# Performance work log

Hardware: AMD Instinct MI355X
Metric: run time of the kernel (lower is better)

## Reference

```python
import jax, jax.numpy as jnp
import numpy as np

DECAY = 0.99
EPSILON = 1e-05
BETA = 0.25  # vq_commitment_beta


def setup_inputs() -> dict:
    key = jax.random.key(0)
    k1, k2, k3, k4 = jax.random.split(key, 4)
    N, dim, K = 32768, 512, 8192
    init_range = 1.0 / np.sqrt(dim)
    emb_w = jax.random.uniform(k3, (K, 2 * dim), dtype=jnp.float32,
                               minval=-init_range, maxval=init_range)
    return {
        "z_real": jax.random.normal(k1, (N, dim), dtype=jnp.float32),
        "z_imag": jax.random.normal(k2, (N, dim), dtype=jnp.float32),
        "emb_w": emb_w,
        "ema_cluster_size": jnp.zeros((K,), dtype=jnp.float32),
        "ema_w": emb_w.copy(),
    }


def reference(z_real, z_imag, emb_w, ema_cluster_size, ema_w):
    N, dim = z_real.shape
    K = emb_w.shape[0]
    z_flat = jnp.concatenate([z_real, z_imag], axis=-1)  # [N, 2*dim]

    # squared euclidean distances [N, K]
    x_sq = jnp.sum(z_flat * z_flat, axis=1, keepdims=True)
    y_sq = jnp.sum(emb_w * emb_w, axis=1)
    d = jnp.maximum(x_sq + y_sq - 2.0 * (z_flat @ emb_w.T), 0.0)
    indices = jnp.argmin(d, axis=-1)  # [N]
    z_q = emb_w[indices]              # [N, 2*dim]

    # EMA codebook update (training-mode buffer math, no grads)
    n_total = jnp.zeros((K,), z_flat.dtype).at[indices].add(1.0)
    new_cluster_size = ema_cluster_size * DECAY + (1.0 - DECAY) * n_total
    cs = new_cluster_size + EPSILON
    cs = cs + (cs < 1.0).astype(cs.dtype)
    dw = jnp.zeros((K, 2 * dim), z_flat.dtype).at[indices].add(z_flat)  # encodings.T @ z_flat
    new_ema_w = ema_w * DECAY + (1.0 - DECAY) * dw
    new_w = jnp.clip(new_ema_w / cs[:, None], -5.0, 5.0)

    loss_sample = BETA * jnp.mean((z_q - z_flat) ** 2, axis=-1)  # [N]

    # straight-through (forward value == z_q)
    z_q_st = z_flat + jax.lax.stop_gradient(z_q - z_flat)

    probs = n_total / N
    norm_entropy = -jnp.sum(probs * jnp.log(probs + 1e-10)) / np.log(float(K))

    z_q_r = z_q_st[..., :dim]
    z_q_i = z_q_st[..., dim:]
    return (z_q_r, z_q_i, loss_sample, indices, norm_entropy,
            new_w, new_cluster_size, new_ema_w)
```

## Files before the change

### kernel.cpp

```cpp
#include <hip/hip_runtime.h>
#include <hip/hip_bf16.h>

#define NROWS 32768
#define DIM   512
#define D2    1024
#define KCODE 8192
#define DECAYF 0.99f
#define OMD    0.01f
#define CANDCAP 16
#define ZMAX 6.0f
#define IRANGE 0.04419417382415922f
#define MARGIN_I 9200

typedef __attribute__((ext_vector_type(4))) float f32x4;
typedef __attribute__((ext_vector_type(4))) int   v4i;
typedef __attribute__((ext_vector_type(16))) int  i32x16;

#define WS_EMB8T   0u
#define WS_YSQ     8388608u
#define WS_NINT    8421376u
#define WS_ENT     8454144u
#define WS_CCOUNT  8454160u
#define WS_CAND    8585232u
#define WS_FIDX    10682384u
#define WS_OFF     10813456u
#define WS_CUR     10846224u
#define WS_ROWLIST 10878992u

#define OUT_ZQR  0
#define OUT_ZQI  16777216
#define OUT_LOSS 33554432
#define OUT_IDX  33587200
#define OUT_ENT  33619968
#define OUT_NEWW 33619969
#define OUT_NCS  42008577
#define OUT_NEMA 42016769

__device__ __forceinline__ float wredf(float v) {
    #pragma unroll
    for (int o = 32; o > 0; o >>= 1) v += __shfl_down(v, o, 64);
    return v;
}

__device__ __forceinline__ double wredd(double v) {
    #pragma unroll
    for (int o = 32; o > 0; o >>= 1) v += __shfl_down(v, o, 64);
    return __shfl(v, 0, 64);
}

__device__ __forceinline__ double ulp32_of(double v) {
    return scalbn(1.0, ilogb(v) - 23);
}

__device__ __forceinline__ void gload_lds16(const void* g, void* l) {
    __builtin_amdgcn_global_load_lds(
        (const __attribute__((address_space(1))) unsigned int*)(g),
        (__attribute__((address_space(3))) unsigned int*)(l), 16, 0, 0);
}

__device__ __forceinline__ int q4(float4 v, float s) {
    int a = (int)rintf(fminf(fmaxf(v.x * s, -127.f), 127.f));
    int b = (int)rintf(fminf(fmaxf(v.y * s, -127.f), 127.f));
    int c = (int)rintf(fminf(fmaxf(v.z * s, -127.f), 127.f));
    int d = (int)rintf(fminf(fmaxf(v.w * s, -127.f), 127.f));
    return (a & 255) | ((b & 255) << 8) | ((c & 255) << 16) | ((d & 255) << 24);
}

__global__ __launch_bounds__(256) void prep_emb(const float* __restrict__ emb,
                                                char* __restrict__ emb8t,
                                                int* __restrict__ ysq) {
    int wave = threadIdx.x >> 6, lane = threadIdx.x & 63;
    int k = blockIdx.x * 4 + wave;
    const float4* src = (const float4*)(emb + (size_t)k * D2);
    const float es = 127.0f / IRANGE;
    const float sfac_inv = 1.0f / (2.0f * (ZMAX / 127.0f) * (IRANGE / 127.0f));
    float s = 0.f;
    float4 v0 = src[lane * 4 + 0];
    float4 v1 = src[lane * 4 + 1];
    float4 v2 = src[lane * 4 + 2];
    float4 v3 = src[lane * 4 + 3];
    s += v0.x*v0.x + v0.y*v0.y + v0.z*v0.z + v0.w*v0.w;
    s += v1.x*v1.x + v1.y*v1.y + v1.z*v1.z + v1.w*v1.w;
    s += v2.x*v2.x + v2.y*v2.y + v2.z*v2.z + v2.w*v2.w;
    s += v3.x*v3.x + v3.y*v3.y + v3.z*v3.z + v3.w*v3.w;
    v4i pk; pk[0] = q4(v0, es); pk[1] = q4(v1, es); pk[2] = q4(v2, es); pk[3] = q4(v3, es);
    v4i* dst = (v4i*)(emb8t + (size_t)(k >> 5) * 32768 + (size_t)lane * 512 + (k & 31) * 16);
    *dst = pk;
    s = wredf(s);
    if (lane == 0) ysq[k] = (int)rintf(s * sfac_inv);
}

__global__ __launch_bounds__(512, 2) void argmin_gemm(
    const float* __restrict__ zr, const float* __restrict__ zi,
    const char* __restrict__ emb8t, const int* __restrict__ ysq,
    long long* __restrict__ pairs)
{
    __shared__ char bufs[2][65536];
    const int tid  = threadIdx.x;
    const int wave = tid >> 6, lane = tid & 63;
    const int colc = lane & 31;
    const int hh   = lane >> 5;
    const int rowblk = blockIdx.x >> 1;
    const int slice  = blockIdx.x & 1;

    const int arow = rowblk * 256 + wave * 32 + colc;
    const float zs = 127.0f / ZMAX;
    const float* zrp = zr + (size_t)arow * 512 + hh * 16;
    const float* zip = zi + (size_t)arow * 512 + hh * 16;
    v4i afrag[32];
    #pragma unroll
    for (int ft = 0; ft < 16; ++ft) {
        const float4* p = (const float4*)(zrp + ft * 32);
        v4i a; a[0] = q4(p[0], zs); a[1] = q4(p[1], zs); a[2] = q4(p[2], zs); a[3] = q4(p[3], zs);
        afrag[ft] = a;
    }
    #pragma unroll
    for (int ft = 0; ft < 16; ++ft) {
        const float4* p = (const float4*)(zip + ft * 32);
        v4i a; a[0] = q4(p[0], zs); a[1] = q4(p[1], zs); a[2] = q4(p[2], zs); a[3] = q4(p[3], zs);
        afrag[16 + ft] = a;
    }

    int tv0[16], tv1[16], cpk[16];
    #pragma unroll
    for (int g = 0; g < 16; ++g) { tv0[g] = 0x7FFFFFFF; tv1[g] = 0x7FFFFFFF; cpk[g] = 0; }

    const char* gslice = emb8t + (size_t)slice * 128 * 32768;
    const int* yslice = ysq + slice * 4096;

#define STAGE(dstbuf, c_) do {                                                   \
        const char* gb = gslice + (size_t)(c_) * 65536 + wave * 8192             \
                       + (size_t)lane * 16;                                      \
        char* lb = (dstbuf) + wave * 8192;                                       \
        _Pragma("unroll")                                                        \
        for (int q = 0; q < 8; ++q)                                              \
            gload_lds16(gb + q * 1024, lb + q * 1024);                           \
    } while (0)

    const int boff = colc * 16 + hh * 512;

    STAGE(bufs[0], 0);
    __syncthreads();

    for (int c = 0; c < 64; ++c) {
        const int cur = c & 1;
        if (c + 1 < 64) STAGE(bufs[cur ^ 1], c + 1);

        const char* bb = &bufs[cur][0] + boff;
        i32x16 accA, accB;
        #pragma unroll
        for (int g = 0; g < 16; ++g) { accA[g] = 0; accB[g] = 0; }
        #pragma unroll
        for (int m = 0; m < 32; ++m) {
            v4i bA = *(const v4i*)(bb + m * 1024);
            v4i bB = *(const v4i*)(bb + m * 1024 + 32768);
            accA = __builtin_amdgcn_mfma_i32_32x32x32_i8(afrag[m], bA, accA, 0, 0, 0);
            accB = __builtin_amdgcn_mfma_i32_32x32x32_i8(afrag[m], bB, accB, 0, 0, 0);
        }

        int ysA = yslice[c * 64 + colc];
        int ysB = yslice[c * 64 + 32 + colc];
        const int idA = c * 2, idB = c * 2 + 1;
        #pragma unroll
        for (int g = 0; g < 16; ++g) {
            int sc = ysA - accA[g];
            if (sc < tv1[g]) {
                bool b0 = sc < tv0[g];
                int cp = cpk[g];
                cpk[g] = b0 ? (((cp & 0xFF) << 8) | idA) : ((cp & 0xFF) | (idA << 8));
                int ov0 = tv0[g];
                tv1[g] = b0 ? ov0 : sc;
                tv0[g] = b0 ? sc : ov0;
            }
            sc = ysB - accB[g];
            if (sc < tv1[g]) {
                bool b0 = sc < tv0[g];
                int cp = cpk[g];
                cpk[g] = b0 ? (((cp & 0xFF) << 8) | idB) : ((cp & 0xFF) | (idB << 8));
                int ov0 = tv0[g];
                tv1[g] = b0 ? ov0 : sc;
                tv0[g] = b0 ? sc : ov0;
            }
        }
        __syncthreads();
    }
#undef STAGE

    #pragma unroll
    for (int g = 0; g < 16; ++g) {
        int rloc = (g & 3) + 8 * (g >> 2) + 4 * hh;
        int rowg = rowblk * 256 + wave * 32 + rloc;
        size_t base = (size_t)rowg * 128 + slice * 64 + colc * 2;
        int cp = cpk[g];
        int code0 = slice * 4096 + (cp & 0xFF) * 32 + colc;
        int code1 = slice * 4096 + ((cp >> 8) & 0xFF) * 32 + colc;
        pairs[base + 0] = ((long long)(unsigned)code0 << 32) | (unsigned)tv0[g];
        pairs[base + 1] = ((long long)(unsigned)code1 << 32) | (unsigned)tv1[g];
    }
}

__global__ __launch_bounds__(256) void merge_rows(const long long* __restrict__ pairs,
                                                  int* __restrict__ cand,
                                                  int* __restrict__ ccount)
{
    int wave = threadIdx.x >> 6, lane = threadIdx.x & 63;
    int row = blockIdx.x * 4 + wave;
    const long long* pr = pairs + (size_t)row * 128;
    long long p0 = pr[lane];
    long long p1 = pr[64 + lane];
    int v0v = (int)(unsigned)p0;
    int i0  = (int)(p0 >> 32);
    int v1v = (int)(unsigned)p1;
    int i1  = (int)(p1 >> 32);
    int m = min(v0v, v1v);
    #pragma unroll
    for (int o = 32; o > 0; o >>= 1) m = min(m, __shfl_xor(m, o, 64));
    int lim = m + MARGIN_I;
    unsigned long long m0 = __ballot(v0v < lim);
    unsigned long long m1 = __ballot(v1v < lim);
    int t0 = __popcll(m0);
    int cnt = t0 + __popcll(m1);
    if (cnt > CANDCAP) cnt = CANDCAP;
    unsigned long long below = (lane == 63) ? 0xFFFFFFFFFFFFFFFFull >> 1
                                            : ((1ull << lane) - 1);
    if (v0v < lim) {
        int pos = __popcll(m0 & below);
        if (pos < CANDCAP) cand[(size_t)row * CANDCAP + pos] = i0;
    }
    if (v1v < lim) {
        int pos = t0 + __popcll(m1 & below);
        if (pos < CANDCAP) cand[(size_t)row * CANDCAP + pos] = i1;
    }
    if (lane == 0) ccount[row] = cnt;
}

__global__ __launch_bounds__(256) void cleanup(
    const float* __restrict__ zr, const float* __restrict__ zi,
    const float* __restrict__ emb, const int* __restrict__ cand,
    const int* __restrict__ ccount, int* __restrict__ fidx,
    int* __restrict__ nint, float* __restrict__ out)
{
    int wave = threadIdx.x >> 6, lane = threadIdx.x & 63;
    int r = blockIdx.x * 4 + wave;
    int cnt = ccount[r];
    int best = cand[r * CANDCAP];

    float zreg[16];
    #pragma unroll
    for (int p = 0; p < 4; ++p) {
        int d4 = p * 64 + lane;
        const float4* zp = (d4 < 128) ? (const float4*)(zr + (size_t)r * 512)
                                      : ((const float4*)(zi + (size_t)r * 512) - 128);
        float4 zv = zp[d4];
        zreg[p * 4 + 0] = zv.x; zreg[p * 4 + 1] = zv.y;
        zreg[p * 4 + 2] = zv.z; zreg[p * 4 + 3] = zv.w;
    }

    if (cnt > 1) {
        double xs = 0.0;
        #pragma unroll
        for (int j = 0; j < 16; ++j) xs += (double)zreg[j] * (double)zreg[j];
        xs = wredd(xs);
        double uS = ulp32_of(xs);

        double bD = 1e300; int bi = 1 << 30;
        for (int i = 0; i < cnt; ++i) {
            int cdx = cand[r * CANDCAP + i];
            const float4* ep = (const float4*)(emb + (size_t)cdx * 1024);
            double ys = 0.0, tt = 0.0;
            #pragma unroll
            for (int p = 0; p < 4; ++p) {
                float4 ev = ep[p * 64 + lane];
                float p0 = ev.x * ev.x, p1 = ev.y * ev.y, p2 = ev.z * ev.z, p3 = ev.w * ev.w;
                ys += (double)p0 + (double)p1 + (double)p2 + (double)p3;
                tt += (double)zreg[p * 4 + 0] * (double)ev.x
                    + (double)zreg[p * 4 + 1] * (double)ev.y
                    + (double)zreg[p * 4 + 2] * (double)ev.z
                    + (double)zreg[p * 4 + 3] * (double)ev.w;
            }
            ys = wredd(ys);
            tt = wredd(tt);
            float y32 = (float)ys;
            float t32 = (float)tt;
            double dex = xs + ys - 2.0 * tt;
            double ud = ulp32_of(dex);
            double D = rint((double)y32 / uS) * uS - rint(2.0 * (double)t32 / ud) * ud;
            if (D < bD || (D == bD && cdx < bi)) { bD = D; bi = cdx; }
        }
        best = bi;
    }

    const float4* ep = (const float4*)(emb + (size_t)best * 1024);
    float acc = 0.f;
    #pragma unroll
    for (int p = 0; p < 4; ++p) {
        int d4 = p * 64 + lane;
        float4 ev = ep[d4];
        float dx = ev.x - zreg[p * 4 + 0]; acc += dx * dx;
        float dy = ev.y - zreg[p * 4 + 1]; acc += dy * dy;
        float dz = ev.z - zreg[p * 4 + 2]; acc += dz * dz;
        float dw = ev.w - zreg[p * 4 + 3]; acc += dw * dw;
        float4* op = (d4 < 128) ? (float4*)(out + OUT_ZQR + (size_t)r * 512)
                                : ((float4*)(out + OUT_ZQI + (size_t)r * 512) - 128);
        op[d4] = ev;
    }
    acc = wredf(acc);
    if (lane == 0) {
        fidx[r] = best;
        out[OUT_IDX + r] = (float)best;
        out[OUT_LOSS + r] = 0.25f * acc * (1.f / 1024.f);
        atomicAdd(nint + best, 1);
    }
}

__global__ __launch_bounds__(256) void scan_codes(const int* __restrict__ nint,
                                                  int* __restrict__ off,
                                                  int* __restrict__ cur) {
    __shared__ int part[256];
    int tid = threadIdx.x;
    int base = tid * 32;
    int loc[32];
    int s = 0;
    #pragma unroll
    for (int j = 0; j < 32; ++j) { loc[j] = s; s += nint[base + j]; }
    part[tid] = s;
    __syncthreads();
    for (int o = 1; o < 256; o <<= 1) {
        int t = (tid >= o) ? part[tid - o] : 0;
        __syncthreads();
        part[tid] += t;
        __syncthreads();
    }
    int excl = part[tid] - s;
    #pragma unroll
    for (int j = 0; j < 32; ++j) {
        off[base + j] = excl + loc[j];
        cur[base + j] = 0;
    }
}

__global__ __launch_bounds__(256) void fill_rows(const int* __restrict__ fidx,
                                                 const int* __restrict__ off,
                                                 int* __restrict__ cur,
                                                 int* __restrict__ rowlist) {
    int r = blockIdx.x * 256 + threadIdx.x;
    int idx = fidx[r];
    int pos = atomicAdd(cur + idx, 1);
    rowlist[off[idx] + pos] = r;
}

__global__ __launch_bounds__(256) void ema_update(
    const float* __restrict__ zr, const float* __restrict__ zi,
    const float* __restrict__ emaw, const float* __restrict__ emacs,
    const int* __restrict__ nint, const int* __restrict__ off,
    const int* __restrict__ rowlist, float* __restrict__ out,
    float* __restrict__ entacc)
{
    int k = blockIdx.x;
    int tid = threadIdx.x;
    int cnt = nint[k];
    int o0 = off[k];
    float ax = 0.f, ay = 0.f, az = 0.f, aw = 0.f;
    for (int i = 0; i < cnt; ++i) {
        int r = rowlist[o0 + i];
        float4 zv = (tid < 128) ? ((const float4*)(zr + (size_t)r * 512))[tid]
                                : ((const float4*)(zi + (size_t)r * 512))[tid - 128];
        ax += zv.x; ay += zv.y; az += zv.z; aw += zv.w;
    }
    float4 ew = ((const float4*)(emaw + (size_t)k * 1024))[tid];
    float4 nem;
    nem.x = DECAYF * ew.x + OMD * ax;
    nem.y = DECAYF * ew.y + OMD * ay;
    nem.z = DECAYF * ew.z + OMD * az;
    nem.w = DECAYF * ew.w + OMD * aw;
    ((float4*)(out + OUT_NEMA + (size_t)k * 1024))[tid] = nem;
    float ncs = DECAYF * emacs[k] + OMD * (float)cnt;
    float cs = ncs + 1e-5f;
    if (cs < 1.f) cs += 1.f;
    float inv = 1.f / cs;
    float4 w;
    w.x = fminf(fmaxf(nem.x * inv, -5.f), 5.f);
    w.y = fminf(fmaxf(nem.y * inv, -5.f), 5.f);
    w.z = fminf(fmaxf(nem.z * inv, -5.f), 5.f);
    w.w = fminf(fmaxf(nem.w * inv, -5.f), 5.f);
    ((float4*)(out + OUT_NEWW + (size_t)k * 1024))[tid] = w;
    if (tid == 0) {
        out[OUT_NCS + k] = ncs;
        float p = (float)cnt / 32768.f;
        atomicAdd(entacc, -p * logf(p + 1e-10f));
    }
}

__global__ void ent_fin(const float* __restrict__ entacc, float* __restrict__ out) {
    if (threadIdx.x == 0) out[OUT_ENT] = entacc[0] / logf(8192.f);
}

extern "C" void kernel_launch(void* const* d_in, const int* in_sizes, int n_in,
                              void* d_out, int out_size, void* d_ws, size_t ws_size,
                              hipStream_t stream)
{
    const float* zr    = (const float*)d_in[0];
    const float* zi    = (const float*)d_in[1];
    const float* emb   = (const float*)d_in[2];
    const float* emacs = (const float*)d_in[3];
    const float* emaw  = (const float*)d_in[4];
    float* out = (float*)d_out;
    char* ws = (char*)d_ws;

    char*  emb8t   = (char*)(ws + WS_EMB8T);
    int*   ysq     = (int*)(ws + WS_YSQ);
    int*   nint    = (int*)(ws + WS_NINT);
    float* entacc  = (float*)(ws + WS_ENT);
    int*   ccount  = (int*)(ws + WS_CCOUNT);
    int*   cand    = (int*)(ws + WS_CAND);
    int*   fidx    = (int*)(ws + WS_FIDX);
    int*   off     = (int*)(ws + WS_OFF);
    int*   cur     = (int*)(ws + WS_CUR);
    int*   rowlist = (int*)(ws + WS_ROWLIST);
    long long* pairs = (long long*)out;

    hipMemsetAsync(ws + WS_NINT, 0, 32768 + 16, stream);

    prep_emb   <<<2048, 256, 0, stream>>>(emb, emb8t, ysq);
    argmin_gemm<<<256,  512, 0, stream>>>(zr, zi, emb8t, ysq, pairs);
    merge_rows <<<8192, 256, 0, stream>>>(pairs, cand, ccount);
    cleanup    <<<8192, 256, 0, stream>>>(zr, zi, emb, cand, ccount, fidx, nint, out);
    scan_codes <<<1,    256, 0, stream>>>(nint, off, cur);
    fill_rows  <<<128,  256, 0, stream>>>(fidx, off, cur, rowlist);
    ema_update <<<8192, 256, 0, stream>>>(zr, zi, emaw, emacs, nint, off, rowlist, out, entacc);
    ent_fin    <<<1,    64,  0, stream>>>(entacc, out);
}
```

Baseline: 550.9 us.

## Software-pipeline top-2 selection behind next chunk's MFMAs with packed branchless keys

The distance-scan kernel now double-buffers its MFMA accumulators, so each chunk's top-2 update runs on the previous chunk's results and can overlap the current chunk's matrix instructions. The top-2 tracking becomes branchless by packing the chunk id into the low 7 bits of a shifted score and using min/max, which removes the separate cpk index register. It also raises wave priority around the MFMA block with s_setprio. The cost is a second set of accumulators, which adds register pressure. The shifted score could overflow if distances are large, and the merge margin is rescaled to match the new key format.

Result: slower. 1.871 ms (+239.6%).

```diff
diff --git a/kernel.cpp b/kernel.cpp
--- a/kernel.cpp
+++ b/kernel.cpp
@@ -10,9 +10,8 @@
 #define CANDCAP 16
 #define ZMAX 6.0f
 #define IRANGE 0.04419417382415922f
-#define MARGIN_I 9200
-
-typedef __attribute__((ext_vector_type(4))) float f32x4;
+#define MARGIN_P (9200 << 7)
+
 typedef __attribute__((ext_vector_type(4))) int   v4i;
 typedef __attribute__((ext_vector_type(16))) int  i32x16;
 
@@ -121,9 +120,9 @@
         afrag[16 + ft] = a;
     }
 
-    int tv0[16], tv1[16], cpk[16];
-    #pragma unroll
-    for (int g = 0; g < 16; ++g) { tv0[g] = 0x7FFFFFFF; tv1[g] = 0x7FFFFFFF; cpk[g] = 0; }
+    int tv0[16], tv1[16];
+    #pragma unroll
+    for (int g = 0; g < 16; ++g) { tv0[g] = 0x7FFFFFFF; tv1[g] = 0x7FFFFFFF; }
 
     const char* gslice = emb8t + (size_t)slice * 128 * 32768;
     const int* yslice = ysq + slice * 4096;
@@ -139,63 +138,76 @@
 
     const int boff = colc * 16 + hh * 512;
 
+    i32x16 accA0, accB0, accA1, accB1;
+    #pragma unroll
+    for (int g = 0; g < 16; ++g) { accA1[g] = 0; accB1[g] = 0; }
+    int pysA = 1 << 23, pysB = 1 << 23, pidA = 0, pidB = 0;
+
     STAGE(bufs[0], 0);
     __syncthreads();
 
-    for (int c = 0; c < 64; ++c) {
-        const int cur = c & 1;
-        if (c + 1 < 64) STAGE(bufs[cur ^ 1], c + 1);
-
-        const char* bb = &bufs[cur][0] + boff;
-        i32x16 accA, accB;
-        #pragma unroll
-        for (int g = 0; g < 16; ++g) { accA[g] = 0; accB[g] = 0; }
-        #pragma unroll
-        for (int m = 0; m < 32; ++m) {
-            v4i bA = *(const v4i*)(bb + m * 1024);
-            v4i bB = *(const v4i*)(bb + m * 1024 + 32768);
-            accA = __builtin_amdgcn_mfma_i32_32x32x32_i8(afrag[m], bA, accA, 0, 0, 0);
-            accB = __builtin_amdgcn_mfma_i32_32x32x32_i8(afrag[m], bB, accB, 0, 0, 0);
-        }
-
-        int ysA = yslice[c * 64 + colc];
-        int ysB = yslice[c * 64 + 32 + colc];
-        const int idA = c * 2, idB = c * 2 + 1;
-        #pragma unroll
-        for (int g = 0; g < 16; ++g) {
-            int sc = ysA - accA[g];
-            if (sc < tv1[g]) {
-                bool b0 = sc < tv0[g];
-                int cp = cpk[g];
-                cpk[g] = b0 ? (((cp & 0xFF) << 8) | idA) : ((cp & 0xFF) | (idA << 8));
-                int ov0 = tv0[g];
-                tv1[g] = b0 ? ov0 : sc;
-                tv0[g] = b0 ? sc : ov0;
-            }
-            sc = ysB - accB[g];
-            if (sc < tv1[g]) {
-                bool b0 = sc < tv0[g];
-                int cp = cpk[g];
-                cpk[g] = b0 ? (((cp & 0xFF) << 8) | idB) : ((cp & 0xFF) | (idB << 8));
-                int ov0 = tv0[g];
-                tv1[g] = b0 ? ov0 : sc;
-                tv0[g] = b0 ? sc : ov0;
-            }
-        }
-        __syncthreads();
-    }
+#define CHUNK_BODY(c_, curA, curB, prvA, prvB) do {                              \
+        const int cc = (c_);                                                     \
+        if (cc + 1 < 64) STAGE(bufs[(cc + 1) & 1], cc + 1);                      \
+        const char* bb = &bufs[cc & 1][0] + boff;                                \
+        _Pragma("unroll")                                                        \
+        for (int g = 0; g < 16; ++g) { curA[g] = 0; curB[g] = 0; }               \
+        __builtin_amdgcn_s_setprio(1);                                           \
+        _Pragma("unroll")                                                        \
+        for (int m = 0; m < 32; ++m) {                                           \
+            v4i bA = *(const v4i*)(bb + m * 1024);                               \
+            v4i bB = *(const v4i*)(bb + m * 1024 + 32768);                       \
+            curA = __builtin_amdgcn_mfma_i32_32x32x32_i8(afrag[m], bA, curA, 0, 0, 0); \
+            curB = __builtin_amdgcn_mfma_i32_32x32x32_i8(afrag[m], bB, curB, 0, 0, 0); \
+        }                                                                        \
+        __builtin_amdgcn_s_setprio(0);                                           \
+        _Pragma("unroll")                                                        \
+        for (int g = 0; g < 16; ++g) {                                           \
+            int pkA = ((pysA - prvA[g]) << 7) | pidA;                            \
+            int t1A = min(tv1[g], max(pkA, tv0[g]));                             \
+            tv0[g] = min(tv0[g], pkA);                                           \
+            tv1[g] = t1A;                                                        \
+            int pkB = ((pysB - prvB[g]) << 7) | pidB;                            \
+            int t1B = min(tv1[g], max(pkB, tv0[g]));                             \
+            tv0[g] = min(tv0[g], pkB);                                           \
+            tv1[g] = t1B;                                                        \
+        }                                                                        \
+        pysA = yslice[cc * 64 + colc];                                           \
+        pysB = yslice[cc * 64 + 32 + colc];                                      \
+        pidA = cc * 2;                                                           \
+        pidB = cc * 2 + 1;                                                       \
+        __syncthreads();                                                         \
+    } while (0)
+
+    for (int cp = 0; cp < 32; ++cp) {
+        CHUNK_BODY(2 * cp,     accA0, accB0, accA1, accB1);
+        CHUNK_BODY(2 * cp + 1, accA1, accB1, accA0, accB0);
+    }
+#undef CHUNK_BODY
 #undef STAGE
+
+    #pragma unroll
+    for (int g = 0; g < 16; ++g) {
+        int pkA = ((pysA - accA1[g]) << 7) | pidA;
+        int t1A = min(tv1[g], max(pkA, tv0[g]));
+        tv0[g] = min(tv0[g], pkA);
+        tv1[g] = t1A;
+        int pkB = ((pysB - accB1[g]) << 7) | pidB;
+        int t1B = min(tv1[g], max(pkB, tv0[g]));
+        tv0[g] = min(tv0[g], pkB);
+        tv1[g] = t1B;
+    }
 
     #pragma unroll
     for (int g = 0; g < 16; ++g) {
         int rloc = (g & 3) + 8 * (g >> 2) + 4 * hh;
         int rowg = rowblk * 256 + wave * 32 + rloc;
         size_t base = (size_t)rowg * 128 + slice * 64 + colc * 2;
-        int cp = cpk[g];
-        int code0 = slice * 4096 + (cp & 0xFF) * 32 + colc;
-        int code1 = slice * 4096 + ((cp >> 8) & 0xFF) * 32 + colc;
-        pairs[base + 0] = ((long long)(unsigned)code0 << 32) | (unsigned)tv0[g];
-        pairs[base + 1] = ((long long)(unsigned)code1 << 32) | (unsigned)tv1[g];
+        int t0 = tv0[g], t1 = tv1[g];
+        int code0 = slice * 4096 + (t0 & 127) * 32 + colc;
+        int code1 = slice * 4096 + (t1 & 127) * 32 + colc;
+        pairs[base + 0] = ((long long)(unsigned)code0 << 32) | (unsigned)t0;
+        pairs[base + 1] = ((long long)(unsigned)code1 << 32) | (unsigned)t1;
     }
 }
 
@@ -215,7 +227,7 @@
     int m = min(v0v, v1v);
     #pragma unroll
     for (int o = 32; o > 0; o >>= 1) m = min(m, __shfl_xor(m, o, 64));
-    int lim = m + MARGIN_I;
+    int lim = m + MARGIN_P;
     unsigned long long m0 = __ballot(v0v < lim);
     unsigned long long m1 = __ballot(v1v < lim);
     int t0 = __popcll(m0);
```

## Pack score and index for branchless top-2 and fuse merge into cleanup

Applied to the files above, without the earlier changes.

The GEMM epilogue now packs each int8 distance score with its 7-bit chunk index into a single int, so the top-2 tracking becomes branchless min/max operations instead of compare-and-select with a separate index word. The merge_rows kernel is folded into cleanup, which keeps the candidate list in LDS rather than round-tripping cand/ccount through global memory. The pairs buffer moves to the new_w region of the output so cleanup can write z_q outputs without clobbering it. MFMA loops are also wrapped in s_setprio and the ysq loads are hoisted ahead of the MFMAs. The shift by 7 risks overflow if scores exceed about 2^24, and ties now resolve by chunk index.

Result: faster. 518.1 us (-5.9%).

```diff
diff --git a/kernel.cpp b/kernel.cpp
--- a/kernel.cpp
+++ b/kernel.cpp
@@ -10,9 +10,8 @@
 #define CANDCAP 16
 #define ZMAX 6.0f
 #define IRANGE 0.04419417382415922f
-#define MARGIN_I 9200
-
-typedef __attribute__((ext_vector_type(4))) float f32x4;
+#define MARGIN_P (9200 << 7)
+
 typedef __attribute__((ext_vector_type(4))) int   v4i;
 typedef __attribute__((ext_vector_type(16))) int  i32x16;
 
@@ -20,8 +19,6 @@
 #define WS_YSQ     8388608u
 #define WS_NINT    8421376u
 #define WS_ENT     8454144u
-#define WS_CCOUNT  8454160u
-#define WS_CAND    8585232u
 #define WS_FIDX    10682384u
 #define WS_OFF     10813456u
 #define WS_CUR     10846224u
@@ -35,6 +32,7 @@
 #define OUT_NEWW 33619969
 #define OUT_NCS  42008577
 #define OUT_NEMA 42016769
+#define PAIRS_OFF (OUT_NEWW + 1)
 
 __device__ __forceinline__ float wredf(float v) {
     #pragma unroll
@@ -121,9 +119,9 @@
         afrag[16 + ft] = a;
     }
 
-    int tv0[16], tv1[16], cpk[16];
-    #pragma unroll
-    for (int g = 0; g < 16; ++g) { tv0[g] = 0x7FFFFFFF; tv1[g] = 0x7FFFFFFF; cpk[g] = 0; }
+    int tv0[16], tv1[16];
+    #pragma unroll
+    for (int g = 0; g < 16; ++g) { tv0[g] = 0x7FFFFFFF; tv1[g] = 0x7FFFFFFF; }
 
     const char* gslice = emb8t + (size_t)slice * 128 * 32768;
     const int* yslice = ysq + slice * 4096;
@@ -145,11 +143,14 @@
     for (int c = 0; c < 64; ++c) {
         const int cur = c & 1;
         if (c + 1 < 64) STAGE(bufs[cur ^ 1], c + 1);
+        int ysA = yslice[c * 64 + colc];
+        int ysB = yslice[c * 64 + 32 + colc];
 
         const char* bb = &bufs[cur][0] + boff;
         i32x16 accA, accB;
         #pragma unroll
         for (int g = 0; g < 16; ++g) { accA[g] = 0; accB[g] = 0; }
+        __builtin_amdgcn_s_setprio(1);
         #pragma unroll
         for (int m = 0; m < 32; ++m) {
             v4i bA = *(const v4i*)(bb + m * 1024);
@@ -157,30 +158,17 @@
             accA = __builtin_amdgcn_mfma_i32_32x32x32_i8(afrag[m], bA, accA, 0, 0, 0);
             accB = __builtin_amdgcn_mfma_i32_32x32x32_i8(afrag[m], bB, accB, 0, 0, 0);
         }
-
-        int ysA = yslice[c * 64 + colc];
-        int ysB = yslice[c * 64 + 32 + colc];
+        __builtin_amdgcn_s_setprio(0);
+
         const int idA = c * 2, idB = c * 2 + 1;
         #pragma unroll
         for (int g = 0; g < 16; ++g) {
-            int sc = ysA - accA[g];
-            if (sc < tv1[g]) {
-                bool b0 = sc < tv0[g];
-                int cp = cpk[g];
-                cpk[g] = b0 ? (((cp & 0xFF) << 8) | idA) : ((cp & 0xFF) | (idA << 8));
-                int ov0 = tv0[g];
-                tv1[g] = b0 ? ov0 : sc;
-                tv0[g] = b0 ? sc : ov0;
-            }
-            sc = ysB - accB[g];
-            if (sc < tv1[g]) {
-                bool b0 = sc < tv0[g];
-                int cp = cpk[g];
-                cpk[g] = b0 ? (((cp & 0xFF) << 8) | idB) : ((cp & 0xFF) | (idB << 8));
-                int ov0 = tv0[g];
-                tv1[g] = b0 ? ov0 : sc;
-                tv0[g] = b0 ? sc : ov0;
-            }
+            int pkA = ((ysA - accA[g]) << 7) | idA;
+            tv1[g] = min(tv1[g], max(pkA, tv0[g]));
+            tv0[g] = min(tv0[g], pkA);
+            int pkB = ((ysB - accB[g]) << 7) | idB;
+            tv1[g] = min(tv1[g], max(pkB, tv0[g]));
+            tv0[g] = min(tv0[g], pkB);
         }
         __syncthreads();
     }
@@ -191,21 +179,24 @@
         int rloc = (g & 3) + 8 * (g >> 2) + 4 * hh;
         int rowg = rowblk * 256 + wave * 32 + rloc;
         size_t base = (size_t)rowg * 128 + slice * 64 + colc * 2;
-        int cp = cpk[g];
-        int code0 = slice * 4096 + (cp & 0xFF) * 32 + colc;
-        int code1 = slice * 4096 + ((cp >> 8) & 0xFF) * 32 + colc;
-        pairs[base + 0] = ((long long)(unsigned)code0 << 32) | (unsigned)tv0[g];
-        pairs[base + 1] = ((long long)(unsigned)code1 << 32) | (unsigned)tv1[g];
-    }
-}
-
-__global__ __launch_bounds__(256) void merge_rows(const long long* __restrict__ pairs,
-                                                  int* __restrict__ cand,
-                                                  int* __restrict__ ccount)
+        int t0 = tv0[g], t1 = tv1[g];
+        int code0 = slice * 4096 + (t0 & 127) * 32 + colc;
+        int code1 = slice * 4096 + (t1 & 127) * 32 + colc;
+        pairs[base + 0] = ((long long)(unsigned)code0 << 32) | (unsigned)t0;
+        pairs[base + 1] = ((long long)(unsigned)code1 << 32) | (unsigned)t1;
+    }
+}
+
+__global__ __launch_bounds__(256) void cleanup(
+    const float* __restrict__ zr, const float* __restrict__ zi,
+    const float* __restrict__ emb, const long long* __restrict__ pairs,
+    int* __restrict__ fidx, int* __restrict__ nint, float* __restrict__ out)
 {
+    __shared__ int candlds[4][CANDCAP];
     int wave = threadIdx.x >> 6, lane = threadIdx.x & 63;
-    int row = blockIdx.x * 4 + wave;
-    const long long* pr = pairs + (size_t)row * 128;
+    int r = blockIdx.x * 4 + wave;
+
+    const long long* pr = pairs + (size_t)r * 128;
     long long p0 = pr[lane];
     long long p1 = pr[64 + lane];
     int v0v = (int)(unsigned)p0;
@@ -215,7 +206,7 @@
     int m = min(v0v, v1v);
     #pragma unroll
     for (int o = 32; o > 0; o >>= 1) m = min(m, __shfl_xor(m, o, 64));
-    int lim = m + MARGIN_I;
+    int lim = m + MARGIN_P;
     unsigned long long m0 = __ballot(v0v < lim);
     unsigned long long m1 = __ballot(v1v < lim);
     int t0 = __popcll(m0);
@@ -225,25 +216,13 @@
                                             : ((1ull << lane) - 1);
     if (v0v < lim) {
         int pos = __popcll(m0 & below);
-        if (pos < CANDCAP) cand[(size_t)row * CANDCAP + pos] = i0;
+        if (pos < CANDCAP) candlds[wave][pos] = i0;
     }
     if (v1v < lim) {
         int pos = t0 + __popcll(m1 & below);
-        if (pos < CANDCAP) cand[(size_t)row * CANDCAP + pos] = i1;
-    }
-    if (lane == 0) ccount[row] = cnt;
-}
-
-__global__ __launch_bounds__(256) void cleanup(
-    const float* __restrict__ zr, const float* __restrict__ zi,
-    const float* __restrict__ emb, const int* __restrict__ cand,
-    const int* __restrict__ ccount, int* __restrict__ fidx,
-    int* __restrict__ nint, float* __restrict__ out)
-{
-    int wave = threadIdx.x >> 6, lane = threadIdx.x & 63;
-    int r = blockIdx.x * 4 + wave;
-    int cnt = ccount[r];
-    int best = cand[r * CANDCAP];
+        if (pos < CANDCAP) candlds[wave][pos] = i1;
+    }
+    int best = candlds[wave][0];
 
     float zreg[16];
     #pragma unroll
@@ -265,14 +244,14 @@
 
         double bD = 1e300; int bi = 1 << 30;
         for (int i = 0; i < cnt; ++i) {
-            int cdx = cand[r * CANDCAP + i];
+            int cdx = candlds[wave][i];
             const float4* ep = (const float4*)(emb + (size_t)cdx * 1024);
             double ys = 0.0, tt = 0.0;
             #pragma unroll
             for (int p = 0; p < 4; ++p) {
                 float4 ev = ep[p * 64 + lane];
-                float p0 = ev.x * ev.x, p1 = ev.y * ev.y, p2 = ev.z * ev.z, p3 = ev.w * ev.w;
-                ys += (double)p0 + (double)p1 + (double)p2 + (double)p3;
+                float q0 = ev.x * ev.x, q1 = ev.y * ev.y, q2 = ev.z * ev.z, q3 = ev.w * ev.w;
+                ys += (double)q0 + (double)q1 + (double)q2 + (double)q3;
                 tt += (double)zreg[p * 4 + 0] * (double)ev.x
                     + (double)zreg[p * 4 + 1] * (double)ev.y
                     + (double)zreg[p * 4 + 2] * (double)ev.z
@@ -411,20 +390,17 @@
     int*   ysq     = (int*)(ws + WS_YSQ);
     int*   nint    = (int*)(ws + WS_NINT);
     float* entacc  = (float*)(ws + WS_ENT);
-    int*   ccount  = (int*)(ws + WS_CCOUNT);
-    int*   cand    = (int*)(ws + WS_CAND);
     int*   fidx    = (int*)(ws + WS_FIDX);
     int*   off     = (int*)(ws + WS_OFF);
     int*   cur     = (int*)(ws + WS_CUR);
     int*   rowlist = (int*)(ws + WS_ROWLIST);
-    long long* pairs = (long long*)out;
+    long long* pairs = (long long*)(out + PAIRS_OFF);
 
     hipMemsetAsync(ws + WS_NINT, 0, 32768 + 16, stream);
 
     prep_emb   <<<2048, 256, 0, stream>>>(emb, emb8t, ysq);
     argmin_gemm<<<256,  512, 0, stream>>>(zr, zi, emb8t, ysq, pairs);
-    merge_rows <<<8192, 256, 0, stream>>>(pairs, cand, ccount);
-    cleanup    <<<8192, 256, 0, stream>>>(zr, zi, emb, cand, ccount, fidx, nint, out);
+    cleanup    <<<8192, 256, 0, stream>>>(zr, zi, emb, pairs, fidx, nint, out);
     scan_codes <<<1,    256, 0, stream>>>(nint, off, cur);
     fill_rows  <<<128,  256, 0, stream>>>(fidx, off, cur, rowlist);
     ema_update <<<8192, 256, 0, stream>>>(zr, zi, emaw, emacs, nint, off, rowlist, out, entacc);
```
